# Kernel tuning notes

Measured on AMD Instinct MI355X. Metric: run time of the kernel, lower is better.

The kernel has to match this reference:

```python
import jax, jax.numpy as jnp
import numpy as np

N = 50000          # nodes
E_EDGES = 800000   # edges (before self loops)
IN_F = 256
HEADS = 4
OUT_F = 64
NEG_SLOPE = 0.2    # PyG GATv2Conv default negative_slope
EPS_GN = 1e-5      # GraphNorm eps


def setup_inputs() -> dict:
    key = jax.random.key(0)
    ks = jax.random.split(key, 8)
    X = jax.random.normal(ks[0], (N, IN_F), jnp.float32)
    E = jax.random.randint(ks[1], (2, E_EDGES), 0, N, jnp.int32)
    s_in = 1.0 / np.sqrt(IN_F)
    Wl = jax.random.normal(ks[2], (IN_F, HEADS * OUT_F), jnp.float32) * s_in   # lin_l (source)
    Wr = jax.random.normal(ks[3], (IN_F, HEADS * OUT_F), jnp.float32) * s_in   # lin_r (target)
    att = jax.random.normal(ks[4], (HEADS, OUT_F), jnp.float32) / np.sqrt(OUT_F)
    bias = jnp.zeros((OUT_F,), jnp.float32)           # concat=False -> bias of size out_channels
    gn_weight = jnp.ones((OUT_F,), jnp.float32)       # GraphNorm gamma
    gn_bias = jnp.zeros((OUT_F,), jnp.float32)        # GraphNorm beta
    gn_mean_scale = jnp.ones((OUT_F,), jnp.float32)   # GraphNorm alpha
    return {"X": X, "E": E, "Wl": Wl, "Wr": Wr, "att": att, "bias": bias,
            "gn_weight": gn_weight, "gn_bias": gn_bias, "gn_mean_scale": gn_mean_scale}


def reference(X, E, Wl, Wr, att, bias, gn_weight, gn_bias, gn_mean_scale):
    # --- GATv2Conv (heads=HEADS, concat=False, add_self_loops=True, eval: no dropout) ---
    loop = jnp.arange(N, dtype=E.dtype)
    src = jnp.concatenate([E[0], loop])   # [Et]
    dst = jnp.concatenate([E[1], loop])   # [Et]
    xl = (X @ Wl).reshape(N, HEADS, OUT_F)  # source transform
    xr = (X @ Wr).reshape(N, HEADS, OUT_F)  # target transform
    # per-edge attention logits: a^T LeakyReLU(xl_j + xr_i)
    e = jax.nn.leaky_relu(xl[src] + xr[dst], NEG_SLOPE)        # [Et, H, C]
    logits = jnp.einsum('ehc,hc->eh', e, att)                  # [Et, H]
    # segment softmax over incoming edges of each destination node
    m = jax.lax.stop_gradient(jax.ops.segment_max(logits, dst, num_segments=N))
    p = jnp.exp(logits - m[dst])
    denom = jax.ops.segment_sum(p, dst, num_segments=N)
    alpha = p / (denom[dst] + 1e-16)                           # [Et, H]
    out = jax.ops.segment_sum(xl[src] * alpha[:, :, None], dst, num_segments=N)  # [N, H, C]
    out = out.mean(axis=1) + bias                              # concat=False -> mean over heads
    # --- GraphNorm (single graph) ---
    mu = out.mean(axis=0)
    xc = out - gn_mean_scale * mu
    var = (xc * xc).mean(axis=0)
    return gn_weight * xc * jax.lax.rsqrt(var + EPS_GN) + gn_bias
```

## Files before the change

### kernel.cpp

```cpp
#include <hip/hip_runtime.h>
#include <hip/hip_bf16.h>

#define IN_F   256
#define HEADS  4
#define OUT_F  64
#define HF     (HEADS * OUT_F)
#define NOUT   512
#define MAXDEG 128

typedef __bf16 bf16x8 __attribute__((ext_vector_type(8)));
typedef float  f32x4  __attribute__((ext_vector_type(4)));
typedef float  f32x2  __attribute__((ext_vector_type(2)));

__device__ __forceinline__ unsigned short f2bf(float f) {
    unsigned u = __float_as_uint(f);
    return (unsigned short)((u + 0x7FFFu + ((u >> 16) & 1u)) >> 16);
}
__device__ __forceinline__ void gld_lds16(const unsigned short* g, unsigned short* lds_base) {
    __builtin_amdgcn_global_load_lds(
        (const __attribute__((address_space(1))) unsigned int*)g,
        (__attribute__((address_space(3))) unsigned int*)lds_base,
        16, 0, 0);
}
__device__ __forceinline__ f32x2 up2(int u) {
    f32x2 r;
    r.x = __uint_as_float(((unsigned)u) << 16);
    r.y = __uint_as_float(((unsigned)u) & 0xFFFF0000u);
    return r;
}
__device__ __forceinline__ f32x2 max2(f32x2 a, f32x2 b) {
    f32x2 r; r.x = fmaxf(a.x, b.x); r.y = fmaxf(a.y, b.y); return r;
}

__global__ __launch_bounds__(256) void prep(
    const float* __restrict__ X, const float* __restrict__ Wl,
    const float* __restrict__ Wr, const int* __restrict__ E,
    unsigned short* __restrict__ Xb, unsigned short* __restrict__ Wt,
    int* __restrict__ deg, int* __restrict__ ssrc,
    int M, int Mp, int EE)
{
    const int b = blockIdx.x, t = threadIdx.x;
    const int idx = b * 256 + t;

    if (idx < Mp * 64) {
        int e = idx * 4;
        int row = e >> 8;
        float4 v = make_float4(0.f, 0.f, 0.f, 0.f);
        if (row < M) v = *(const float4*)(X + e);
        ushort4 o;
        o.x = f2bf(v.x); o.y = f2bf(v.y); o.z = f2bf(v.z); o.w = f2bf(v.w);
        *(ushort4*)(Xb + e) = o;
    }
    if (b < NOUT) {
        const float* W = (b < HF) ? Wl : Wr;
        Wt[b * IN_F + t] = f2bf(W[t * HF + (b & (HF - 1))]);
    }
    int ei = idx * 4;
    if (ei < EE) {
        int4 s4 = *(const int4*)(E + ei);
        int4 d4 = *(const int4*)(E + EE + ei);
        int p0 = atomicAdd(&deg[d4.x], 1);
        int p1 = atomicAdd(&deg[d4.y], 1);
        int p2 = atomicAdd(&deg[d4.z], 1);
        int p3 = atomicAdd(&deg[d4.w], 1);
        if (p0 < MAXDEG) ssrc[d4.x * MAXDEG + p0] = s4.x;
        if (p1 < MAXDEG) ssrc[d4.y * MAXDEG + p1] = s4.y;
        if (p2 < MAXDEG) ssrc[d4.z * MAXDEG + p2] = s4.z;
        if (p3 < MAXDEG) ssrc[d4.w * MAXDEG + p3] = s4.w;
    }
}

__global__ __launch_bounds__(256, 2) void gemm_mfma(
    const unsigned short* __restrict__ Xb,
    const unsigned short* __restrict__ Wt,
    unsigned short* __restrict__ xlr)
{
    __shared__ __align__(16) unsigned short As[128 * 64];
    __shared__ __align__(16) unsigned short Bs[256 * 64];

    const int tid  = threadIdx.x;
    const int w    = tid >> 6;
    const int lane = tid & 63;
    const int m0   = blockIdx.x * 128;
    const int n0   = blockIdx.y * 256;
    const int wm   = (w >> 1) * 64;
    const int wn   = (w & 1) * 128;

    f32x4 acc[4][8];
    #pragma unroll
    for (int i = 0; i < 4; ++i)
        #pragma unroll
        for (int j = 0; j < 8; ++j)
            #pragma unroll
            for (int r = 0; r < 4; ++r) acc[i][j][r] = 0.f;

    const int lr = lane >> 3;
    const int ls = lane & 7;

    for (int k0 = 0; k0 < IN_F; k0 += 64) {
        #pragma unroll
        for (int i = 0; i < 4; ++i) {
            int r = w * 32 + i * 8 + lr;
            int c = ls ^ (r & 7);
            gld_lds16(Xb + (size_t)(m0 + r) * IN_F + k0 + c * 8, &As[(w * 32 + i * 8) * 64]);
        }
        #pragma unroll
        for (int i = 0; i < 8; ++i) {
            int r = w * 64 + i * 8 + lr;
            int c = ls ^ (r & 7);
            gld_lds16(Wt + (size_t)(n0 + r) * IN_F + k0 + c * 8, &Bs[(w * 64 + i * 8) * 64]);
        }
        __syncthreads();

        #pragma unroll
        for (int t = 0; t < 2; ++t) {
            bf16x8 af[4], bfr[8];
            #pragma unroll
            for (int i = 0; i < 4; ++i) {
                int m = wm + i * 16 + (lane & 15);
                int s = (t * 4 + (lane >> 4)) ^ (lane & 7);
                af[i] = __builtin_bit_cast(bf16x8, *(const int4*)&As[m * 64 + s * 8]);
            }
            #pragma unroll
            for (int j = 0; j < 8; ++j) {
                int n = wn + j * 16 + (lane & 15);
                int s = (t * 4 + (lane >> 4)) ^ (lane & 7);
                bfr[j] = __builtin_bit_cast(bf16x8, *(const int4*)&Bs[n * 64 + s * 8]);
            }
            #pragma unroll
            for (int i = 0; i < 4; ++i)
                #pragma unroll
                for (int j = 0; j < 8; ++j)
                    acc[i][j] = __builtin_amdgcn_mfma_f32_16x16x32_bf16(
                        af[i], bfr[j], acc[i][j], 0, 0, 0);
        }
        __syncthreads();
    }

    #pragma unroll
    for (int j = 0; j < 8; ++j) {
        int gc = n0 + wn + j * 16 + (lane & 15);
        #pragma unroll
        for (int i = 0; i < 4; ++i) {
            int gr0 = m0 + wm + i * 16 + (lane >> 4) * 4;
            #pragma unroll
            for (int r = 0; r < 4; ++r)
                xlr[(size_t)(gr0 + r) * NOUT + gc] = f2bf(acc[i][j][r]);
        }
    }
}

__global__ __launch_bounds__(128) void aggr_csr(
    const unsigned short* __restrict__ xlr, const float* __restrict__ att,
    const int* __restrict__ deg, const int* __restrict__ ssrc,
    float* __restrict__ accum, int N)
{
    const int v = blockIdx.x * 2 + (threadIdx.x >> 6);
    if (v >= N) return;
    const int lane = threadIdx.x & 63;
    const int hw = lane >> 5;
    const int h  = (lane >> 3) & 3;
    const int q  = lane & 7;
    const int cbase = h * OUT_F + q * 8;

    const float L2E = 1.44269504088896f;
    f32x2 at2[4];
    {
        float4 a0 = *(const float4*)(att + cbase);
        float4 a1 = *(const float4*)(att + cbase + 4);
        at2[0].x = L2E * a0.x; at2[0].y = L2E * a0.y;
        at2[1].x = L2E * a0.z; at2[1].y = L2E * a0.w;
        at2[2].x = L2E * a1.x; at2[2].y = L2E * a1.y;
        at2[3].x = L2E * a1.z; at2[3].y = L2E * a1.w;
    }
    f32x2 r2[4];
    {
        int4 ru = *(const int4*)(xlr + (size_t)v * NOUT + HF + cbase);
        r2[0] = up2(ru.x); r2[1] = up2(ru.y); r2[2] = up2(ru.z); r2[3] = up2(ru.w);
    }

    f32x2 S0 = {0.f,0.f}, S1 = {0.f,0.f}, S2 = {0.f,0.f}, S3 = {0.f,0.f};
    float den = 0.f;

    const int o0 = v * MAXDEG;
    const int items = deg[v] + 1;
    const unsigned short* xbase = xlr + cbase;

    for (int e0 = 0; e0 < items; e0 += 64) {
        int it = e0 + lane;
        int sv = v;
        if (it > 0 && it < items) sv = ssrc[o0 + it - 1];
        const int nch = min(64, items - e0);
        const int npair = (nch + 1) >> 1;

        int j = 0;
        for (; j + 2 <= npair; j += 2) {
            const int iA = 2 * j + hw, iB = iA + 2;
            const int sA = __shfl(sv, iA, 64);
            const int sB = __shfl(sv, iB, 64);
            int4 uA = *(const int4*)(xbase + (size_t)sA * NOUT);
            int4 uB = *(const int4*)(xbase + (size_t)sB * NOUT);
            f32x2 a0 = up2(uA.x), a1 = up2(uA.y), a2 = up2(uA.z), a3 = up2(uA.w);
            f32x2 b0 = up2(uB.x), b1 = up2(uB.y), b2 = up2(uB.z), b3 = up2(uB.w);
            f32x2 sa0 = a0 + r2[0], sa1 = a1 + r2[1], sa2 = a2 + r2[2], sa3 = a3 + r2[3];
            f32x2 sb0 = b0 + r2[0], sb1 = b1 + r2[1], sb2 = b2 + r2[2], sb3 = b3 + r2[3];
            f32x2 tA2 = max2(sa0, 0.2f * sa0) * at2[0];
            tA2 += max2(sa1, 0.2f * sa1) * at2[1];
            tA2 += max2(sa2, 0.2f * sa2) * at2[2];
            tA2 += max2(sa3, 0.2f * sa3) * at2[3];
            f32x2 tB2 = max2(sb0, 0.2f * sb0) * at2[0];
            tB2 += max2(sb1, 0.2f * sb1) * at2[1];
            tB2 += max2(sb2, 0.2f * sb2) * at2[2];
            tB2 += max2(sb3, 0.2f * sb3) * at2[3];
            float tA = tA2.x + tA2.y, tB = tB2.x + tB2.y;
            tA += __shfl_xor(tA, 1, 64); tB += __shfl_xor(tB, 1, 64);
            tA += __shfl_xor(tA, 2, 64); tB += __shfl_xor(tB, 2, 64);
            tA += __shfl_xor(tA, 4, 64); tB += __shfl_xor(tB, 4, 64);
            float pA = ((e0 + iA) < items) ? exp2f(tA) : 0.f;
            float pB = ((e0 + iB) < items) ? exp2f(tB) : 0.f;
            den += pA + pB;
            S0 += pA * a0 + pB * b0;
            S1 += pA * a1 + pB * b1;
            S2 += pA * a2 + pB * b2;
            S3 += pA * a3 + pB * b3;
        }
        for (; j < npair; ++j) {
            const int iA = 2 * j + hw;
            const int sA = __shfl(sv, iA, 64);
            int4 uA = *(const int4*)(xbase + (size_t)sA * NOUT);
            f32x2 a0 = up2(uA.x), a1 = up2(uA.y), a2 = up2(uA.z), a3 = up2(uA.w);
            f32x2 sa0 = a0 + r2[0], sa1 = a1 + r2[1], sa2 = a2 + r2[2], sa3 = a3 + r2[3];
            f32x2 tA2 = max2(sa0, 0.2f * sa0) * at2[0];
            tA2 += max2(sa1, 0.2f * sa1) * at2[1];
            tA2 += max2(sa2, 0.2f * sa2) * at2[2];
            tA2 += max2(sa3, 0.2f * sa3) * at2[3];
            float tA = tA2.x + tA2.y;
            tA += __shfl_xor(tA, 1, 64);
            tA += __shfl_xor(tA, 2, 64);
            tA += __shfl_xor(tA, 4, 64);
            float pA = ((e0 + iA) < items) ? exp2f(tA) : 0.f;
            den += pA;
            S0 += pA * a0; S1 += pA * a1; S2 += pA * a2; S3 += pA * a3;
        }
    }

    den += __shfl_xor(den, 32, 64);
    S0.x += __shfl_xor(S0.x, 32, 64); S0.y += __shfl_xor(S0.y, 32, 64);
    S1.x += __shfl_xor(S1.x, 32, 64); S1.y += __shfl_xor(S1.y, 32, 64);
    S2.x += __shfl_xor(S2.x, 32, 64); S2.y += __shfl_xor(S2.y, 32, 64);
    S3.x += __shfl_xor(S3.x, 32, 64); S3.y += __shfl_xor(S3.y, 32, 64);

    const float inv = 1.f / (den + 1e-16f);
    float o[8] = { S0.x*inv, S0.y*inv, S1.x*inv, S1.y*inv,
                   S2.x*inv, S2.y*inv, S3.x*inv, S3.y*inv };
    #pragma unroll
    for (int k = 0; k < 8; ++k) {
        o[k] += __shfl_xor(o[k], 8, 64);
        o[k] += __shfl_xor(o[k], 16, 64);
        o[k] *= 0.25f;
    }
    if (lane < 8) {
        float* dst = accum + (size_t)v * OUT_F + lane * 8;
        *(float4*)(dst)     = make_float4(o[0], o[1], o[2], o[3]);
        *(float4*)(dst + 4) = make_float4(o[4], o[5], o[6], o[7]);
    }
}

__global__ __launch_bounds__(256) void gn_stats(
    const float* __restrict__ accum, const float* __restrict__ bias,
    float* __restrict__ gsum, float* __restrict__ gsumsq, int total)
{
    const int tid = threadIdx.x;
    const int col = tid & 63;
    const float b = bias[col];
    float s = 0.f, s2 = 0.f;
    for (int idx = blockIdx.x * 256 + tid; idx < total; idx += gridDim.x * 256) {
        float o = accum[idx] + b;
        s += o; s2 += o * o;
    }
    __shared__ float ls[4][64], ls2[4][64];
    const int w = tid >> 6;
    ls[w][col] = s; ls2[w][col] = s2;
    __syncthreads();
    if (tid < 64) {
        atomicAdd(&gsum[tid],   ls[0][tid] + ls[1][tid] + ls[2][tid] + ls[3][tid]);
        atomicAdd(&gsumsq[tid], ls2[0][tid] + ls2[1][tid] + ls2[2][tid] + ls2[3][tid]);
    }
}

__global__ __launch_bounds__(256) void gn_norm(
    const float* __restrict__ accum, const float* __restrict__ bias,
    const float* __restrict__ gsum, const float* __restrict__ gsumsq,
    const float* __restrict__ gw, const float* __restrict__ gb,
    const float* __restrict__ gms,
    float* __restrict__ out, int total, float invN)
{
    const int idx = blockIdx.x * 256 + threadIdx.x;
    if (idx >= total) return;
    const int col = idx & 63;
    float mu = gsum[col] * invN;
    float m2 = gsumsq[col] * invN;
    float a  = gms[col];
    float var = m2 - 2.f * a * mu * mu + a * a * mu * mu;
    float o  = accum[idx] + bias[col];
    float xc = o - a * mu;
    out[idx] = gw[col] * xc * rsqrtf(var + 1e-5f) + gb[col];
}

extern "C" void kernel_launch(void* const* d_in, const int* in_sizes, int n_in,
                              void* d_out, int out_size, void* d_ws, size_t ws_size,
                              hipStream_t stream)
{
    const float* X    = (const float*)d_in[0];
    const int*   E    = (const int*)  d_in[1];
    const float* Wl   = (const float*)d_in[2];
    const float* Wr   = (const float*)d_in[3];
    const float* att  = (const float*)d_in[4];
    const float* bias = (const float*)d_in[5];
    const float* gw   = (const float*)d_in[6];
    const float* gb   = (const float*)d_in[7];
    const float* gms  = (const float*)d_in[8];
    float* out = (float*)d_out;

    const int N  = in_sizes[0] / IN_F;
    const int EE = in_sizes[1] / 2;
    const int total = N * OUT_F;
    const int MT = (N + 127) / 128;
    const int Mp = MT * 128;

    char* ws = (char*)d_ws;
    unsigned short* Xb  = (unsigned short*)ws;
    unsigned short* Wt  = Xb + (size_t)Mp * IN_F;
    unsigned short* xlr = Wt + (size_t)NOUT * IN_F;
    int*   deg    = (int*)(xlr + (size_t)Mp * NOUT);
    float* gsum   = (float*)(deg + N);
    float* gsumsq = gsum + 64;
    int*   ssrc   = (int*)(gsumsq + 64);
    float* accum  = (float*)(ssrc + (size_t)N * MAXDEG);

    hipMemsetAsync(deg, 0, ((size_t)N + 128) * 4, stream);

    prep<<<(Mp * 64 + 255) / 256, 256, 0, stream>>>(
        X, Wl, Wr, E, Xb, Wt, deg, ssrc, N, Mp, EE);

    dim3 ggrid(MT, 2);
    gemm_mfma<<<ggrid, 256, 0, stream>>>(Xb, Wt, xlr);

    aggr_csr<<<(N + 1) / 2, 128, 0, stream>>>(xlr, att, deg, ssrc, accum, N);

    gn_stats<<<1024, 256, 0, stream>>>(accum, bias, gsum, gsumsq, total);
    gn_norm<<<(total + 255) / 256, 256, 0, stream>>>(
        accum, bias, gsum, gsumsq, gw, gb, gms, out, total, 1.0f / (float)N);
}
```

Baseline: 275.1 us.

## Move edge scatter into GEMM kernel as extra blocks to overlap with MFMA work

The edge-to-CSR scatter (atomic degree counting and source-list writes) is taken out of the prep kernel. It now runs as a leading set of blocks inside the GEMM launch, and the GEMM grid is flattened to 1D with an offset. The aim is to overlap the memory- and atomic-bound scatter with the compute-bound MFMA GEMM, and to keep prep from being slowed by atomics. The scatter blocks still reserve the GEMM's large LDS allocation, which can limit how many of them run at once.

After: 266.8 us. 1.03x faster.

```diff
diff --git a/kernel.cpp b/kernel.cpp
--- a/kernel.cpp
+++ b/kernel.cpp
@@ -34,10 +34,9 @@
 
 __global__ __launch_bounds__(256) void prep(
     const float* __restrict__ X, const float* __restrict__ Wl,
-    const float* __restrict__ Wr, const int* __restrict__ E,
+    const float* __restrict__ Wr,
     unsigned short* __restrict__ Xb, unsigned short* __restrict__ Wt,
-    int* __restrict__ deg, int* __restrict__ ssrc,
-    int M, int Mp, int EE)
+    int M, int Mp)
 {
     const int b = blockIdx.x, t = threadIdx.x;
     const int idx = b * 256 + t;
@@ -55,10 +54,23 @@
         const float* W = (b < HF) ? Wl : Wr;
         Wt[b * IN_F + t] = f2bf(W[t * HF + (b & (HF - 1))]);
     }
-    int ei = idx * 4;
-    if (ei < EE) {
-        int4 s4 = *(const int4*)(E + ei);
-        int4 d4 = *(const int4*)(E + EE + ei);
+}
+
+__global__ __launch_bounds__(256, 2) void gemm_scatter(
+    const unsigned short* __restrict__ Xb,
+    const unsigned short* __restrict__ Wt,
+    unsigned short* __restrict__ xlr,
+    const int* __restrict__ E, int* __restrict__ deg,
+    int* __restrict__ ssrc, int EE, int SB)
+{
+    __shared__ __align__(16) unsigned short As[128 * 64];
+    __shared__ __align__(16) unsigned short Bs[256 * 64];
+
+    if (blockIdx.x < SB) {
+        int i = (blockIdx.x * 256 + threadIdx.x) * 4;
+        if (i >= EE) return;
+        int4 s4 = *(const int4*)(E + i);
+        int4 d4 = *(const int4*)(E + EE + i);
         int p0 = atomicAdd(&deg[d4.x], 1);
         int p1 = atomicAdd(&deg[d4.y], 1);
         int p2 = atomicAdd(&deg[d4.z], 1);
@@ -67,22 +79,15 @@
         if (p1 < MAXDEG) ssrc[d4.y * MAXDEG + p1] = s4.y;
         if (p2 < MAXDEG) ssrc[d4.z * MAXDEG + p2] = s4.z;
         if (p3 < MAXDEG) ssrc[d4.w * MAXDEG + p3] = s4.w;
-    }
-}
-
-__global__ __launch_bounds__(256, 2) void gemm_mfma(
-    const unsigned short* __restrict__ Xb,
-    const unsigned short* __restrict__ Wt,
-    unsigned short* __restrict__ xlr)
-{
-    __shared__ __align__(16) unsigned short As[128 * 64];
-    __shared__ __align__(16) unsigned short Bs[256 * 64];
-
+        return;
+    }
+
+    const int g    = blockIdx.x - SB;
     const int tid  = threadIdx.x;
     const int w    = tid >> 6;
     const int lane = tid & 63;
-    const int m0   = blockIdx.x * 128;
-    const int n0   = blockIdx.y * 256;
+    const int m0   = (g >> 1) * 128;
+    const int n0   = (g & 1) * 256;
     const int wm   = (w >> 1) * 64;
     const int wn   = (w & 1) * 128;
 
@@ -327,6 +332,7 @@
     const int total = N * OUT_F;
     const int MT = (N + 127) / 128;
     const int Mp = MT * 128;
+    const int SB = (EE / 4 + 255) / 256;
 
     char* ws = (char*)d_ws;
     unsigned short* Xb  = (unsigned short*)ws;
@@ -340,11 +346,9 @@
 
     hipMemsetAsync(deg, 0, ((size_t)N + 128) * 4, stream);
 
-    prep<<<(Mp * 64 + 255) / 256, 256, 0, stream>>>(
-        X, Wl, Wr, E, Xb, Wt, deg, ssrc, N, Mp, EE);
-
-    dim3 ggrid(MT, 2);
-    gemm_mfma<<<ggrid, 256, 0, stream>>>(Xb, Wt, xlr);
+    prep<<<(Mp * 64 + 255) / 256, 256, 0, stream>>>(X, Wl, Wr, Xb, Wt, N, Mp);
+
+    gemm_scatter<<<SB + 2 * MT, 256, 0, stream>>>(Xb, Wt, xlr, E, deg, ssrc, EE, SB);
 
     aggr_csr<<<(N + 1) / 2, 128, 0, stream>>>(xlr, att, deg, ssrc, accum, N);
 
```
